# Kernel tuning notes

Hardware: AMD Instinct MI355X
Metric: run time of the kernel (lower is better)

Reference implementation:

```python
import jax, jax.numpy as jnp
import numpy as np

B, N, S, K, CIN = 16, 4096, 1024, 32, 64
EPS = 1e-5


def setup_inputs() -> dict:
    key = jax.random.key(0)
    ks = jax.random.split(key, 6)
    xyz = jax.random.normal(ks[0], (B, N, 3), jnp.float32)
    features = jax.random.normal(ks[1], (B, N, CIN), jnp.float32)
    # random sampling without replacement (mirrors torch.randperm(N)[:npoint])
    fps_idx = jax.vmap(lambda k: jax.random.permutation(k, N)[:S])(
        jax.random.split(ks[2], B)).astype(jnp.int32)
    chans = [CIN + 3, 64, 64, 128]
    params = {}
    for i in range(3):
        cin, cout = chans[i], chans[i + 1]
        params[f"W{i}"] = jax.random.normal(ks[3 + i], (cout, cin), jnp.float32) / np.sqrt(cin).astype(np.float32)
        params[f"b{i}"] = jnp.zeros((cout,), jnp.float32)
        params[f"g{i}"] = jnp.ones((cout,), jnp.float32)
        params[f"bt{i}"] = jnp.zeros((cout,), jnp.float32)
    return dict(xyz=xyz, features=features, fps_idx=fps_idx, **params)


def _mlp_layer(x, W, b, g, bt):
    # x: (B*S, Cin, K); Conv1d(kernel=1) + BatchNorm1d (training stats) + ReLU
    y = jnp.einsum('oc,bck->bok', W, x) + b[None, :, None]
    mu = y.mean(axis=(0, 2), keepdims=True)
    var = y.var(axis=(0, 2), keepdims=True)  # biased var, as in BN normalization
    y = (y - mu) * jax.lax.rsqrt(var + EPS) * g[None, :, None] + bt[None, :, None]
    return jax.nn.relu(y)


def reference(xyz, features, fps_idx, W0, b0, g0, bt0, W1, b1, g1, bt1, W2, b2, g2, bt2):
    # sample centers: (B, S, 3)
    new_xyz = jnp.take_along_axis(xyz, fps_idx[..., None], axis=1)
    # squared pairwise distances (B, S, N)
    d = (jnp.sum(new_xyz * new_xyz, -1)[..., None]
         + jnp.sum(xyz * xyz, -1)[:, None, :]
         - 2.0 * jnp.einsum('bsd,bnd->bsn', new_xyz, xyz))
    _, idx = jax.lax.top_k(-d, K)  # k nearest -> (B, S, K)
    bidx = jnp.arange(B)[:, None, None]
    g_xyz = xyz[bidx, idx] - new_xyz[:, :, None, :]  # (B, S, K, 3) relative coords
    g_feat = features[bidx, idx]                     # (B, S, K, CIN)
    grouped = jnp.concatenate([g_xyz, g_feat], axis=-1)  # (B, S, K, CIN+3)
    x = grouped.reshape(B * S, K, CIN + 3).transpose(0, 2, 1)  # (B*S, C, K)
    x = _mlp_layer(x, W0, b0, g0, bt0)
    x = _mlp_layer(x, W1, b1, g1, bt1)
    x = _mlp_layer(x, W2, b2, g2, bt2)
    new_features = x.max(axis=-1).reshape(B, S, -1)  # (B, S, 128)
    return new_xyz, new_features
```

## Files before the change

kernel.cpp:

```cpp
#include <hip/hip_runtime.h>
#include <stdint.h>

#define B_   16
#define N_   4096
#define S_   1024
#define K_   32
#define CIN_ 64
#define P_   524288
#define PQ_  16384
#define EPS_ 1e-5f

#define SZ_IDX    ((size_t)P_ * 4)
#define SZ_Y      ((size_t)P_ * 64 * 2)
#define SZ_MX     ((size_t)PQ_ * 128 * 4)
#define OFF_IDX   ((size_t)0)
#define OFF_Y0    (OFF_IDX + SZ_IDX)
#define OFF_Y1    (OFF_Y0 + SZ_Y)
#define OFF_MX    (OFF_Y1 + SZ_Y)
#define OFF_MN    (OFF_MX + SZ_MX)
#define OFF_STATS (OFF_MN + SZ_MX)
#define OFF_FIN   (OFF_STATS + 16384)
#define OFF_FPSC  (OFF_FIN + 2048)
#define WS_NEEDED (OFF_FPSC + (size_t)PQ_ * 4)

typedef unsigned short u16;
typedef short bfrag __attribute__((ext_vector_type(8)));
typedef float f32x4 __attribute__((ext_vector_type(4)));

__device__ __forceinline__ float b2f(unsigned v) {
  return __uint_as_float((v & 0xffffu) << 16);
}
__device__ __forceinline__ u16 f2b(float f) {
  unsigned u = __float_as_uint(f);
  unsigned r = (u + 0x7fffu + ((u >> 16) & 1u)) >> 16;
  return (u16)r;
}
__device__ __forceinline__ unsigned pk2(float a, float b) {
  return (unsigned)f2b(a) | ((unsigned)f2b(b) << 16);
}

__global__ __launch_bounds__(256) void fps_canon_kernel(
    const int* __restrict__ fpsraw, int* __restrict__ fpsc)
{
  __shared__ int is64;
  const int tid = threadIdx.x;
  if (tid == 0) is64 = 1;
  __syncthreads();
  if (tid < 64) {
    if (fpsraw[2 * tid + 1] != 0) atomicAnd(&is64, 0);
  }
  __syncthreads();
  int i = blockIdx.x * 256 + tid;
  if (i < PQ_) {
    int src = is64 ? (2 * i) : i;
    int v = fpsraw[src];
    fpsc[i] = (v & 0xFFF);
  }
}

#define NBIN 2048
#define CAND_CAP 512

__global__ __launch_bounds__(256) void knn_kernel(
    const float* __restrict__ xyz, const int* __restrict__ fps,
    int* __restrict__ idxout, float* __restrict__ out_xyz)
{
  __shared__ unsigned hist[NBIN];
  __shared__ float cd[CAND_CAP];
  __shared__ int   ci_[CAND_CAP];
  __shared__ int   sel[K_];
  __shared__ int   wtot[4];
  __shared__ int   sCnt, sCand, sT;

  const int q   = blockIdx.x;
  const int b   = q >> 10;
  const int tid = threadIdx.x;
  const float* xb = xyz + (size_t)b * N_ * 3;
  const int ctr = fps[q];
  const float cx = xb[ctr*3+0], cy = xb[ctr*3+1], cz = xb[ctr*3+2];

  if (tid == 0) {
    out_xyz[(size_t)q*3+0] = cx;
    out_xyz[(size_t)q*3+1] = cy;
    out_xyz[(size_t)q*3+2] = cz;
    sCnt = 0; sCand = 0;
  }
  for (int i = tid; i < NBIN; i += 256) hist[i] = 0u;
  const float s1 = __fadd_rn(__fadd_rn(__fmul_rn(cx,cx), __fmul_rn(cy,cy)), __fmul_rn(cz,cz));
  __syncthreads();

  float dreg[16];
  #pragma unroll
  for (int it = 0; it < 16; ++it) {
    int n = it * 256 + tid;
    float x0 = xb[n*3+0], x1 = xb[n*3+1], x2 = xb[n*3+2];
    float s2 = __fadd_rn(__fadd_rn(__fmul_rn(x0,x0), __fmul_rn(x1,x1)), __fmul_rn(x2,x2));
    float dt = __fadd_rn(__fadd_rn(__fmul_rn(cx,x0), __fmul_rn(cy,x1)), __fmul_rn(cz,x2));
    float d  = __fsub_rn(__fadd_rn(s1, s2), __fmul_rn(2.0f, dt));
    dreg[it] = d;
    float dc = fmaxf(d, 0.0f);
    int bin = (int)(dc * 128.0f); bin = bin > (NBIN-1) ? (NBIN-1) : bin;
    atomicAdd(&hist[bin], 1u);
  }
  __syncthreads();

  const int base = tid * 8;
  int h[8]; int lsum = 0;
  #pragma unroll
  for (int j = 0; j < 8; ++j) { h[j] = (int)hist[base + j]; lsum += h[j]; }
  const int lane = tid & 63, wid = tid >> 6;
  int scv = lsum;
  #pragma unroll
  for (int off = 1; off < 64; off <<= 1) {
    int v = __shfl_up(scv, off, 64);
    if (lane >= off) scv += v;
  }
  if (lane == 63) wtot[wid] = scv;
  __syncthreads();
  int woff = 0;
  for (int w = 0; w < wid; ++w) woff += wtot[w];
  int run = woff + scv - lsum;
  #pragma unroll
  for (int j = 0; j < 8; ++j) {
    int c = h[j];
    if (run < K_ && run + c >= K_) { sT = base + j; }
    run += c;
  }
  __syncthreads();
  const int T = sT;

  const unsigned long long lmask = (lane == 63) ? 0x7fffffffffffffffull
                                                : ((1ull << lane) - 1ull);
  #pragma unroll
  for (int it = 0; it < 16; ++it) {
    int n = it * 256 + tid;
    float d = dreg[it];
    float dc = fmaxf(d, 0.0f);
    int bin = (int)(dc * 128.0f); bin = bin > (NBIN-1) ? (NBIN-1) : bin;
    bool isSel  = (bin < T);
    bool isCand = (bin == T);
    unsigned long long mSel  = __ballot(isSel);
    unsigned long long mCand = __ballot(isCand);
    int baseS = 0, baseC = 0;
    if (lane == 0) {
      if (mSel)  baseS = atomicAdd(&sCnt,  __popcll(mSel));
      if (mCand) baseC = atomicAdd(&sCand, __popcll(mCand));
    }
    baseS = __shfl(baseS, 0, 64);
    baseC = __shfl(baseC, 0, 64);
    if (isSel) {
      int s = baseS + __popcll(mSel & lmask);
      if (s < K_) sel[s] = n;
    }
    if (isCand) {
      int s = baseC + __popcll(mCand & lmask);
      if (s < CAND_CAP) { cd[s] = d; ci_[s] = n; }
    }
  }
  __syncthreads();

  if (wid == 0) {
    int m = sCnt; m = m > K_ ? K_ : m;
    int cc = sCand; cc = cc > CAND_CAP ? CAND_CAP : cc;
    const int r = K_ - m;
    for (int it = 0; it < r; ++it) {
      float bd = 3.0e38f; int bi = 0x7fffffff;
      for (int j = lane; j < cc; j += 64) {
        float dv = cd[j]; int iv = ci_[j];
        if (dv < bd || (dv == bd && iv < bi)) { bd = dv; bi = iv; }
      }
      #pragma unroll
      for (int off = 32; off > 0; off >>= 1) {
        float od = __shfl_down(bd, off, 64);
        int   oi = __shfl_down(bi, off, 64);
        if (od < bd || (od == bd && oi < bi)) { bd = od; bi = oi; }
      }
      int win = __shfl(bi, 0, 64);
      if (lane == 0) sel[m + it] = win & 0xFFF;
      for (int j = lane; j < cc; j += 64) if (ci_[j] == win) cd[j] = 3.0e38f;
    }
  }
  __syncthreads();
  if (tid < K_) idxout[(size_t)q * K_ + tid] = sel[tid] & 0xFFF;
}


__global__ __launch_bounds__(256) void l0_mfma(
    const float* __restrict__ xyz, const float* __restrict__ feat,
    const int* __restrict__ fps, const int* __restrict__ idxin,
    const float* __restrict__ W0, const float* __restrict__ b0,
    uint4* __restrict__ Y0g, float* __restrict__ sumg, float* __restrict__ sqg)
{
  __shared__ uint4 Wl[12*64];
  __shared__ float bl[64];
  __shared__ float ssum[64], ssq[64];

  const int tid = threadIdx.x;
  const int bid0 = blockIdx.x;
  const int rep = (bid0 & 7) << 9;
  const int bid = (bid0 & 7) * ((int)gridDim.x >> 3) + (bid0 >> 3);
  const int pbase = bid * 128;
  const int q0 = bid * 4;
  const int b = bid >> 8;

  if (tid < 64) { bl[tid] = b0 ? b0[tid] : 0.f; ssum[tid] = 0.f; ssq[tid] = 0.f; }
  for (int u = tid; u < 12*64; u += 256) {
    int kc = u >> 6, o = u & 63;
    unsigned pk[4];
    #pragma unroll
    for (int hh = 0; hh < 4; ++hh) {
      int c0 = kc*8 + hh*2, c1 = c0 + 1;
      float v0 = (c0 < 64) ? W0[o*67 + 3 + c0] : (c0 < 67 ? W0[o*67 + (c0-64)] : 0.f);
      float v1 = (c1 < 64) ? W0[o*67 + 3 + c1] : (c1 < 67 ? W0[o*67 + (c1-64)] : 0.f);
      pk[hh] = pk2(v0, v1);
    }
    Wl[u] = make_uint4(pk[0], pk[1], pk[2], pk[3]);
  }

  const int lane = tid & 63, w = tid >> 6, g = lane >> 4, fr = lane & 15;
  const float* xb = xyz + (size_t)b * N_ * 3;
  const float* fbase = feat + (size_t)b * N_ * 64;

  int pidx[2];
  const int ct = fps[q0 + w] & 0xFFF;
  #pragma unroll
  for (int pm = 0; pm < 2; ++pm)
    pidx[pm] = idxin[pbase + w*32 + pm*16 + fr] & 0xFFF;

  bfrag xv[3][2];
  #pragma unroll
  for (int kk = 0; kk < 3; ++kk) {
    const int kc = kk*4 + g;
    #pragma unroll
    for (int pm = 0; pm < 2; ++pm) {
      uint4 uu;
      if (kc < 8) {
        const float* fp = fbase + pidx[pm]*64 + kc*8;
        float4 fa = *(const float4*)fp;
        float4 fb2 = *(const float4*)(fp + 4);
        uu = make_uint4(pk2(fa.x, fa.y), pk2(fa.z, fa.w),
                        pk2(fb2.x, fb2.y), pk2(fb2.z, fb2.w));
      } else if (kc == 8) {
        int n = pidx[pm];
        float dx = xb[n*3+0] - xb[ct*3+0];
        float dy = xb[n*3+1] - xb[ct*3+1];
        float dz = xb[n*3+2] - xb[ct*3+2];
        uu = make_uint4(pk2(dx, dy), (unsigned)f2b(dz), 0u, 0u);
      } else {
        uu = make_uint4(0u, 0u, 0u, 0u);
      }
      xv[kk][pm] = *(bfrag*)&uu;
    }
  }
  __syncthreads();

  f32x4 acc[4][2];
  #pragma unroll
  for (int m = 0; m < 4; ++m)
    #pragma unroll
    for (int j = 0; j < 4; ++j) {
      float v = bl[m*16 + g*4 + j];
      acc[m][0][j] = v; acc[m][1][j] = v;
    }
  #pragma unroll
  for (int kk = 0; kk < 3; ++kk) {
    const int kc = kk*4 + g;
    bfrag a[4];
    #pragma unroll
    for (int m = 0; m < 4; ++m) { uint4 u = Wl[kc*64 + m*16 + fr]; a[m] = *(bfrag*)&u; }
    #pragma unroll
    for (int m = 0; m < 4; ++m)
      #pragma unroll
      for (int pm = 0; pm < 2; ++pm)
        acc[m][pm] = __builtin_amdgcn_mfma_f32_16x16x32_bf16(a[m], xv[kk][pm], acc[m][pm], 0, 0, 0);
  }

  #pragma unroll
  for (int m = 0; m < 4; ++m) {
    #pragma unroll
    for (int j = 0; j < 4; ++j) {
      float v0 = acc[m][0][j], v1 = acc[m][1][j];
      float s = v0 + v1, s2 = v0*v0 + v1*v1;
      #pragma unroll
      for (int d = 1; d < 16; d <<= 1) { s += __shfl_xor(s, d); s2 += __shfl_xor(s2, d); }
      if (fr == 0) {
        atomicAdd(&ssum[m*16 + g*4 + j], s);
        atomicAdd(&ssq[m*16 + g*4 + j], s2);
      }
    }
    #pragma unroll
    for (int pm = 0; pm < 2; ++pm) {
      unsigned lo = pk2(acc[m][pm][0], acc[m][pm][1]);
      unsigned hi = pk2(acc[m][pm][2], acc[m][pm][3]);
      unsigned plo = (unsigned)__shfl_xor((int)lo, 16, 64);
      unsigned phi = (unsigned)__shfl_xor((int)hi, 16, 64);
      if ((g & 1) == 0) {
        size_t unit = (size_t)(m*2 + (g>>1)) * P_ + pbase + w*32 + pm*16 + fr;
        Y0g[unit] = make_uint4(lo, hi, plo, phi);
      }
    }
  }
  __syncthreads();
  if (tid < 64) { atomicAdd(&sumg[rep + tid], ssum[tid]); atomicAdd(&sqg[rep + tid], ssq[tid]); }
}

__global__ __launch_bounds__(256) void l1_mfma(
    const uint4* __restrict__ Y0g,
    const float* __restrict__ W1, const float* __restrict__ b1,
    const float* __restrict__ sc0, const float* __restrict__ sh0,
    uint4* __restrict__ Y1g, float* __restrict__ sumg, float* __restrict__ sqg)
{
  __shared__ uint4 Wl[8*64];
  __shared__ float scl[64], shl[64], bl[64];
  __shared__ float ssum[64], ssq[64];

  const int tid = threadIdx.x;
  const int bid0 = blockIdx.x;
  const int rep = (bid0 & 7) << 9;
  const int bid = (bid0 & 7) * ((int)gridDim.x >> 3) + (bid0 >> 3);
  const int pbase = bid * 128;

  if (tid < 64) {
    scl[tid] = sc0[tid]; shl[tid] = sh0[tid];
    bl[tid] = b1 ? b1[tid] : 0.f;
    ssum[tid] = 0.f; ssq[tid] = 0.f;
  }
  for (int u = tid; u < 8*64; u += 256) {
    int kc = u >> 6, o = u & 63;
    const float* wp = W1 + o*64 + kc*8;
    float4 wa = *(const float4*)wp;
    float4 wb = *(const float4*)(wp + 4);
    Wl[u] = make_uint4(pk2(wa.x, wa.y), pk2(wa.z, wa.w), pk2(wb.x, wb.y), pk2(wb.z, wb.w));
  }
  __syncthreads();

  const int lane = tid & 63, w = tid >> 6, g = lane >> 4, fr = lane & 15;

  bfrag xv[2][2];
  #pragma unroll
  for (int kk = 0; kk < 2; ++kk) {
    const int kc = kk*4 + g;
    float4 sa = *(const float4*)&scl[kc*8];
    float4 sb = *(const float4*)&scl[kc*8 + 4];
    float4 ha = *(const float4*)&shl[kc*8];
    float4 hb = *(const float4*)&shl[kc*8 + 4];
    #pragma unroll
    for (int pm = 0; pm < 2; ++pm) {
      uint4 yv = Y0g[(size_t)kc * P_ + pbase + w*32 + pm*16 + fr];
      unsigned r0 = pk2(fmaxf(fmaf(sa.x, b2f(yv.x),       ha.x), 0.f),
                        fmaxf(fmaf(sa.y, b2f(yv.x >> 16), ha.y), 0.f));
      unsigned r1 = pk2(fmaxf(fmaf(sa.z, b2f(yv.y),       ha.z), 0.f),
                        fmaxf(fmaf(sa.w, b2f(yv.y >> 16), ha.w), 0.f));
      unsigned r2 = pk2(fmaxf(fmaf(sb.x, b2f(yv.z),       hb.x), 0.f),
                        fmaxf(fmaf(sb.y, b2f(yv.z >> 16), hb.y), 0.f));
      unsigned r3 = pk2(fmaxf(fmaf(sb.z, b2f(yv.w),       hb.z), 0.f),
                        fmaxf(fmaf(sb.w, b2f(yv.w >> 16), hb.w), 0.f));
      uint4 uu = make_uint4(r0, r1, r2, r3);
      xv[kk][pm] = *(bfrag*)&uu;
    }
  }

  f32x4 acc[4][2];
  #pragma unroll
  for (int m = 0; m < 4; ++m)
    #pragma unroll
    for (int j = 0; j < 4; ++j) {
      float v = bl[m*16 + g*4 + j];
      acc[m][0][j] = v; acc[m][1][j] = v;
    }
  #pragma unroll
  for (int kk = 0; kk < 2; ++kk) {
    const int kc = kk*4 + g;
    bfrag a[4];
    #pragma unroll
    for (int m = 0; m < 4; ++m) { uint4 u = Wl[kc*64 + m*16 + fr]; a[m] = *(bfrag*)&u; }
    #pragma unroll
    for (int m = 0; m < 4; ++m)
      #pragma unroll
      for (int pm = 0; pm < 2; ++pm)
        acc[m][pm] = __builtin_amdgcn_mfma_f32_16x16x32_bf16(a[m], xv[kk][pm], acc[m][pm], 0, 0, 0);
  }

  #pragma unroll
  for (int m = 0; m < 4; ++m) {
    #pragma unroll
    for (int j = 0; j < 4; ++j) {
      float v0 = acc[m][0][j], v1 = acc[m][1][j];
      float s = v0 + v1, s2 = v0*v0 + v1*v1;
      #pragma unroll
      for (int d = 1; d < 16; d <<= 1) { s += __shfl_xor(s, d); s2 += __shfl_xor(s2, d); }
      if (fr == 0) {
        atomicAdd(&ssum[m*16 + g*4 + j], s);
        atomicAdd(&ssq[m*16 + g*4 + j], s2);
      }
    }
    #pragma unroll
    for (int pm = 0; pm < 2; ++pm) {
      unsigned lo = pk2(acc[m][pm][0], acc[m][pm][1]);
      unsigned hi = pk2(acc[m][pm][2], acc[m][pm][3]);
      unsigned plo = (unsigned)__shfl_xor((int)lo, 16, 64);
      unsigned phi = (unsigned)__shfl_xor((int)hi, 16, 64);
      if ((g & 1) == 0) {
        size_t unit = (size_t)(m*2 + (g>>1)) * P_ + pbase + w*32 + pm*16 + fr;
        Y1g[unit] = make_uint4(lo, hi, plo, phi);
      }
    }
  }
  __syncthreads();
  if (tid < 64) { atomicAdd(&sumg[rep + tid], ssum[tid]); atomicAdd(&sqg[rep + tid], ssq[tid]); }
}

__global__ __launch_bounds__(256) void l2_mfma(
    const uint4* __restrict__ Y1g,
    const float* __restrict__ W2, const float* __restrict__ b2,
    const float* __restrict__ sc1, const float* __restrict__ sh1,
    float* __restrict__ mxg, float* __restrict__ mng,
    float* __restrict__ sumg, float* __restrict__ sqg)
{
  __shared__ uint4 Wl[8*128];
  __shared__ float scl[64], shl[64], bl[128];
  __shared__ float ssum[128], ssq[128];

  const int tid = threadIdx.x;
  const int bid0 = blockIdx.x;
  const int rep = (bid0 & 7) << 9;
  const int bid = (bid0 & 7) * ((int)gridDim.x >> 3) + (bid0 >> 3);
  const int pbase = bid * 128;
  const int q0 = bid * 4;

  if (tid < 64) { scl[tid] = sc1[tid]; shl[tid] = sh1[tid]; }
  if (tid < 128) { bl[tid] = b2 ? b2[tid] : 0.f; ssum[tid] = 0.f; ssq[tid] = 0.f; }
  for (int u = tid; u < 8*128; u += 256) {
    int kc = u >> 7, o = u & 127;
    const float* wp = W2 + o*64 + kc*8;
    float4 wa = *(const float4*)wp;
    float4 wb = *(const float4*)(wp + 4);
    Wl[u] = make_uint4(pk2(wa.x, wa.y), pk2(wa.z, wa.w), pk2(wb.x, wb.y), pk2(wb.z, wb.w));
  }
  __syncthreads();

  const int lane = tid & 63, w = tid >> 6, g = lane >> 4, fr = lane & 15;

  bfrag ax[2][2];
  #pragma unroll
  for (int kk = 0; kk < 2; ++kk) {
    const int kc = kk*4 + g;
    float4 sa = *(const float4*)&scl[kc*8];
    float4 sb = *(const float4*)&scl[kc*8 + 4];
    float4 ha = *(const float4*)&shl[kc*8];
    float4 hb = *(const float4*)&shl[kc*8 + 4];
    #pragma unroll
    for (int pm = 0; pm < 2; ++pm) {
      uint4 yv = Y1g[(size_t)kc * P_ + pbase + w*32 + pm*16 + fr];
      unsigned r0 = pk2(fmaxf(fmaf(sa.x, b2f(yv.x),       ha.x), 0.f),
                        fmaxf(fmaf(sa.y, b2f(yv.x >> 16), ha.y), 0.f));
      unsigned r1 = pk2(fmaxf(fmaf(sa.z, b2f(yv.y),       ha.z), 0.f),
                        fmaxf(fmaf(sa.w, b2f(yv.y >> 16), ha.w), 0.f));
      unsigned r2 = pk2(fmaxf(fmaf(sb.x, b2f(yv.z),       hb.x), 0.f),
                        fmaxf(fmaf(sb.y, b2f(yv.z >> 16), hb.y), 0.f));
      unsigned r3 = pk2(fmaxf(fmaf(sb.z, b2f(yv.w),       hb.z), 0.f),
                        fmaxf(fmaf(sb.w, b2f(yv.w >> 16), hb.w), 0.f));
      uint4 uu = make_uint4(r0, r1, r2, r3);
      ax[kk][pm] = *(bfrag*)&uu;
    }
  }

  f32x4 acc[2][8];
  #pragma unroll
  for (int cn = 0; cn < 8; ++cn) {
    float v = bl[cn*16 + fr];
    #pragma unroll
    for (int j = 0; j < 4; ++j) { acc[0][cn][j] = v; acc[1][cn][j] = v; }
  }
  #pragma unroll
  for (int kk = 0; kk < 2; ++kk) {
    const int kc = kk*4 + g;
    #pragma unroll
    for (int cn = 0; cn < 8; ++cn) {
      uint4 u = Wl[kc*128 + cn*16 + fr];
      bfrag bw = *(bfrag*)&u;
      acc[0][cn] = __builtin_amdgcn_mfma_f32_16x16x32_bf16(ax[kk][0], bw, acc[0][cn], 0, 0, 0);
      acc[1][cn] = __builtin_amdgcn_mfma_f32_16x16x32_bf16(ax[kk][1], bw, acc[1][cn], 0, 0, 0);
    }
  }

  #pragma unroll
  for (int cn = 0; cn < 8; ++cn) {
    float mx = -3.0e38f, mn = 3.0e38f, s = 0.f, s2 = 0.f;
    #pragma unroll
    for (int pm = 0; pm < 2; ++pm)
      #pragma unroll
      for (int j = 0; j < 4; ++j) {
        float v = acc[pm][cn][j];
        mx = fmaxf(mx, v); mn = fminf(mn, v);
        s += v; s2 += v*v;
      }
    #pragma unroll
    for (int d = 16; d < 64; d <<= 1) {
      mx = fmaxf(mx, __shfl_xor(mx, d));
      mn = fminf(mn, __shfl_xor(mn, d));
      s  += __shfl_xor(s, d);
      s2 += __shfl_xor(s2, d);
    }
    if (g == 0) {
      int o = cn*16 + fr;
      size_t q = q0 + w;
      mxg[q*128 + o] = mx;
      mng[q*128 + o] = mn;
      atomicAdd(&ssum[o], s);
      atomicAdd(&ssq[o], s2);
    }
  }
  __syncthreads();
  if (tid < 128) { atomicAdd(&sumg[rep + tid], ssum[tid]); atomicAdd(&sqg[rep + tid], ssq[tid]); }
}

__global__ void finalize_kernel(
    const float* __restrict__ sum, const float* __restrict__ sq,
    const float* __restrict__ g, const float* __restrict__ bt,
    float* __restrict__ sc, float* __restrict__ sh, int C)
{
  int c = threadIdx.x;
  if (c < C) {
    float s = 0.f, s2 = 0.f;
    #pragma unroll
    for (int r = 0; r < 8; ++r) { s += sum[r*512 + c]; s2 += sq[r*512 + c]; }
    const float inv = 1.0f / (float)P_;
    float mu = s * inv;
    float var = s2 * inv - mu * mu;
    var = fmaxf(var, 0.f);
    float rr = 1.0f / sqrtf(var + EPS_);
    float gg = g ? g[c] : 1.0f;
    float bb = bt ? bt[c] : 0.0f;
    float sv = gg * rr;
    sc[c] = sv;
    sh[c] = bb - mu * sv;
  }
}

__global__ __launch_bounds__(256) void out_kernel(
    const float* __restrict__ mxg, const float* __restrict__ mng,
    const float* __restrict__ sc2, const float* __restrict__ sh2,
    float* __restrict__ out)
{
  int i = blockIdx.x * 256 + threadIdx.x;
  int o = i & 127;
  float a = sc2[o];
  float v = (a >= 0.f) ? mxg[i] : mng[i];
  float z = fmaxf(fmaf(a, v, sh2[o]), 0.f);
  out[(size_t)PQ_ * 3 + i] = z;
}

extern "C" void kernel_launch(void* const* d_in, const int* in_sizes, int n_in,
                              void* d_out, int out_size, void* d_ws, size_t ws_size,
                              hipStream_t stream)
{
  int i_xyz=-1, i_feat=-1, i_fps=-1, i_w0=-1, i_w1=-1, i_w2=-1;
  for (int i = 0; i < n_in; ++i) {
    switch (in_sizes[i]) {
      case 196608:  i_xyz = i; break;
      case 4194304: i_feat = i; break;
      case 16384:   i_fps = i; break;
      case 4288:    i_w0 = i; break;
      case 4096:    i_w1 = i; break;
      case 8192:    i_w2 = i; break;
      default: break;
    }
  }
  if (i_xyz < 0 || i_feat < 0 || i_fps < 0 || i_w0 < 0 || i_w1 < 0 || i_w2 < 0) return;

  const float* xyz  = (const float*)d_in[i_xyz];
  const float* feat = (const float*)d_in[i_feat];
  const int*   fpsr = (const int*)d_in[i_fps];
  const float* W0 = (const float*)d_in[i_w0];
  const float* W1 = (const float*)d_in[i_w1];
  const float* W2 = (const float*)d_in[i_w2];

  bool canon = (n_in >= 15 && i_xyz==0 && i_feat==1 && i_fps==2 && i_w0==3 &&
                i_w1==7 && i_w2==11 &&
                in_sizes[4]==64 && in_sizes[5]==64 && in_sizes[6]==64 &&
                in_sizes[8]==64 && in_sizes[9]==64 && in_sizes[10]==64 &&
                in_sizes[12]==128 && in_sizes[13]==128 && in_sizes[14]==128);
  const float* b0 = canon ? (const float*)d_in[4]  : nullptr;
  const float* g0 = canon ? (const float*)d_in[5]  : nullptr;
  const float* bt0= canon ? (const float*)d_in[6]  : nullptr;
  const float* b1 = canon ? (const float*)d_in[8]  : nullptr;
  const float* g1 = canon ? (const float*)d_in[9]  : nullptr;
  const float* bt1= canon ? (const float*)d_in[10] : nullptr;
  const float* b2 = canon ? (const float*)d_in[12] : nullptr;
  const float* g2 = canon ? (const float*)d_in[13] : nullptr;
  const float* bt2= canon ? (const float*)d_in[14] : nullptr;

  float* out = (float*)d_out;
  char* ws = (char*)d_ws;
  if (ws_size < WS_NEEDED) return;

  int* idxw = (int*)(ws + OFF_IDX);
  uint4* Y0 = (uint4*)(ws + OFF_Y0);
  uint4* Y1 = (uint4*)(ws + OFF_Y1);
  float* mxg = (float*)(ws + OFF_MX);
  float* mng = (float*)(ws + OFF_MN);
  float* st  = (float*)(ws + OFF_STATS);
  float* fin = (float*)(ws + OFF_FIN);
  int* fpsc  = (int*)(ws + OFF_FPSC);

  hipMemsetAsync(st, 0, 16384, stream);

  fps_canon_kernel<<<(PQ_+255)/256, 256, 0, stream>>>(fpsr, fpsc);

  knn_kernel<<<PQ_, 256, 0, stream>>>(xyz, fpsc, idxw, out);

  l0_mfma<<<P_/128, 256, 0, stream>>>(xyz, feat, fpsc, idxw, W0, b0, Y0, st + 0, st + 64);
  finalize_kernel<<<1, 64, 0, stream>>>(st + 0, st + 64, g0, bt0, fin + 0, fin + 64, 64);

  l1_mfma<<<P_/128, 256, 0, stream>>>(Y0, W1, b1, fin + 0, fin + 64, Y1, st + 128, st + 192);
  finalize_kernel<<<1, 64, 0, stream>>>(st + 128, st + 192, g1, bt1, fin + 128, fin + 192, 64);

  l2_mfma<<<P_/128, 256, 0, stream>>>(Y1, W2, b2, fin + 128, fin + 192, mxg, mng, st + 256, st + 384);
  finalize_kernel<<<1, 128, 0, stream>>>(st + 256, st + 384, g2, bt2, fin + 256, fin + 384, 128);

  out_kernel<<<(PQ_*128)/256, 256, 0, stream>>>(mxg, mng, fin + 256, fin + 384, out);
}
```

Measured before the change: 251.2 us.

## Precompute padded xyz with squared norms and streamline KNN histogram threshold search

Adds a prep kernel that packs each point as a float4 of (x,y,z,|p|^2), so the KNN kernel does one aligned 16-byte load per point and skips recomputing the squared norm for every query. The histogram prefix scan becomes a single-wave chunked scan that stops early once the K-th bin is found. Selection and candidate classification now compare distances against float bin bounds instead of recomputing bin indices, and the wave-level atomics are skipped when a ballot mask is empty. The cost is an extra small launch and workspace buffer, plus a serial wave-0 scan that could be slower if the threshold bin lies far along the histogram.

Result: faster. 242.5 us (-3.5%).

```diff
diff --git a/kernel.cpp b/kernel.cpp
--- a/kernel.cpp
+++ b/kernel.cpp
@@ -21,7 +21,8 @@
 #define OFF_STATS (OFF_MN + SZ_MX)
 #define OFF_FIN   (OFF_STATS + 16384)
 #define OFF_FPSC  (OFF_FIN + 2048)
-#define WS_NEEDED (OFF_FPSC + (size_t)PQ_ * 4)
+#define OFF_PXYZW (OFF_FPSC + (size_t)PQ_ * 4)
+#define WS_NEEDED (OFF_PXYZW + (size_t)B_ * N_ * 16)
 
 typedef unsigned short u16;
 typedef short bfrag __attribute__((ext_vector_type(8)));
@@ -58,26 +59,35 @@
   }
 }
 
+__global__ __launch_bounds__(256) void prep_kernel(
+    const float* __restrict__ xyz, float4* __restrict__ pxyzw)
+{
+  int i = blockIdx.x * 256 + threadIdx.x;
+  float x0 = xyz[i*3+0], x1 = xyz[i*3+1], x2 = xyz[i*3+2];
+  float s2 = __fadd_rn(__fadd_rn(__fmul_rn(x0,x0), __fmul_rn(x1,x1)), __fmul_rn(x2,x2));
+  pxyzw[i] = make_float4(x0, x1, x2, s2);
+}
+
 #define NBIN 2048
 #define CAND_CAP 512
 
 __global__ __launch_bounds__(256) void knn_kernel(
-    const float* __restrict__ xyz, const int* __restrict__ fps,
+    const float4* __restrict__ pxyzw, const int* __restrict__ fps,
     int* __restrict__ idxout, float* __restrict__ out_xyz)
 {
   __shared__ unsigned hist[NBIN];
   __shared__ float cd[CAND_CAP];
   __shared__ int   ci_[CAND_CAP];
   __shared__ int   sel[K_];
-  __shared__ int   wtot[4];
   __shared__ int   sCnt, sCand, sT;
 
   const int q   = blockIdx.x;
   const int b   = q >> 10;
   const int tid = threadIdx.x;
-  const float* xb = xyz + (size_t)b * N_ * 3;
+  const float4* xb4 = pxyzw + (size_t)b * N_;
   const int ctr = fps[q];
-  const float cx = xb[ctr*3+0], cy = xb[ctr*3+1], cz = xb[ctr*3+2];
+  const float4 cv = xb4[ctr];
+  const float cx = cv.x, cy = cv.y, cz = cv.z, s1 = cv.w;
 
   if (tid == 0) {
     out_xyz[(size_t)q*3+0] = cx;
@@ -85,18 +95,20 @@
     out_xyz[(size_t)q*3+2] = cz;
     sCnt = 0; sCand = 0;
   }
-  for (int i = tid; i < NBIN; i += 256) hist[i] = 0u;
-  const float s1 = __fadd_rn(__fadd_rn(__fmul_rn(cx,cx), __fmul_rn(cy,cy)), __fmul_rn(cz,cz));
+  {
+    uint4* hz = (uint4*)hist;
+    hz[tid]       = make_uint4(0,0,0,0);
+    hz[tid + 256] = make_uint4(0,0,0,0);
+  }
   __syncthreads();
 
   float dreg[16];
   #pragma unroll
   for (int it = 0; it < 16; ++it) {
     int n = it * 256 + tid;
-    float x0 = xb[n*3+0], x1 = xb[n*3+1], x2 = xb[n*3+2];
-    float s2 = __fadd_rn(__fadd_rn(__fmul_rn(x0,x0), __fmul_rn(x1,x1)), __fmul_rn(x2,x2));
-    float dt = __fadd_rn(__fadd_rn(__fmul_rn(cx,x0), __fmul_rn(cy,x1)), __fmul_rn(cz,x2));
-    float d  = __fsub_rn(__fadd_rn(s1, s2), __fmul_rn(2.0f, dt));
+    float4 v = xb4[n];
+    float dt = __fadd_rn(__fadd_rn(__fmul_rn(cx,v.x), __fmul_rn(cy,v.y)), __fmul_rn(cz,v.z));
+    float d  = __fsub_rn(__fadd_rn(s1, v.w), __fmul_rn(2.0f, dt));
     dreg[it] = d;
     float dc = fmaxf(d, 0.0f);
     int bin = (int)(dc * 128.0f); bin = bin > (NBIN-1) ? (NBIN-1) : bin;
@@ -104,57 +116,60 @@
   }
   __syncthreads();
 
-  const int base = tid * 8;
-  int h[8]; int lsum = 0;
-  #pragma unroll
-  for (int j = 0; j < 8; ++j) { h[j] = (int)hist[base + j]; lsum += h[j]; }
   const int lane = tid & 63, wid = tid >> 6;
-  int scv = lsum;
-  #pragma unroll
-  for (int off = 1; off < 64; off <<= 1) {
-    int v = __shfl_up(scv, off, 64);
-    if (lane >= off) scv += v;
-  }
-  if (lane == 63) wtot[wid] = scv;
-  __syncthreads();
-  int woff = 0;
-  for (int w = 0; w < wid; ++w) woff += wtot[w];
-  int run = woff + scv - lsum;
-  #pragma unroll
-  for (int j = 0; j < 8; ++j) {
-    int c = h[j];
-    if (run < K_ && run + c >= K_) { sT = base + j; }
-    run += c;
+  if (wid == 0) {
+    int cum = 0, base = 0, found = 0;
+    while (!found && base < NBIN) {
+      int h = (int)hist[base + lane];
+      int pre = h;
+      #pragma unroll
+      for (int off = 1; off < 64; off <<= 1) {
+        int v = __shfl_up(pre, off, 64);
+        if (lane >= off) pre += v;
+      }
+      int tot = __shfl(pre, 63, 64);
+      bool cross = (cum + pre >= K_) && (cum + pre - h < K_);
+      unsigned long long mm = __ballot(cross);
+      if (mm) {
+        if (lane == 0) sT = base + (int)(__ffsll((long long)mm) - 1);
+        found = 1;
+      }
+      cum += tot;
+      base += 64;
+    }
   }
   __syncthreads();
   const int T = sT;
+  const float fT  = (float)T * 0.0078125f;
+  const float fT1 = (T >= NBIN-1) ? 3.0e38f : (float)(T+1) * 0.0078125f;
 
   const unsigned long long lmask = (lane == 63) ? 0x7fffffffffffffffull
                                                 : ((1ull << lane) - 1ull);
   #pragma unroll
   for (int it = 0; it < 16; ++it) {
     int n = it * 256 + tid;
-    float d = dreg[it];
-    float dc = fmaxf(d, 0.0f);
-    int bin = (int)(dc * 128.0f); bin = bin > (NBIN-1) ? (NBIN-1) : bin;
-    bool isSel  = (bin < T);
-    bool isCand = (bin == T);
+    float dc = fmaxf(dreg[it], 0.0f);
+    bool isSel  = dc < fT;
+    bool isCand = !isSel && (dc < fT1);
     unsigned long long mSel  = __ballot(isSel);
     unsigned long long mCand = __ballot(isCand);
-    int baseS = 0, baseC = 0;
-    if (lane == 0) {
-      if (mSel)  baseS = atomicAdd(&sCnt,  __popcll(mSel));
-      if (mCand) baseC = atomicAdd(&sCand, __popcll(mCand));
-    }
-    baseS = __shfl(baseS, 0, 64);
-    baseC = __shfl(baseC, 0, 64);
-    if (isSel) {
-      int s = baseS + __popcll(mSel & lmask);
-      if (s < K_) sel[s] = n;
-    }
-    if (isCand) {
-      int s = baseC + __popcll(mCand & lmask);
-      if (s < CAND_CAP) { cd[s] = d; ci_[s] = n; }
+    if (mSel) {
+      int baseS = 0;
+      if (lane == 0) baseS = atomicAdd(&sCnt, __popcll(mSel));
+      baseS = __shfl(baseS, 0, 64);
+      if (isSel) {
+        int s = baseS + __popcll(mSel & lmask);
+        if (s < K_) sel[s] = n;
+      }
+    }
+    if (mCand) {
+      int baseC = 0;
+      if (lane == 0) baseC = atomicAdd(&sCand, __popcll(mCand));
+      baseC = __shfl(baseC, 0, 64);
+      if (isCand) {
+        int s = baseC + __popcll(mCand & lmask);
+        if (s < CAND_CAP) { cd[s] = dreg[it]; ci_[s] = n; }
+      }
     }
   }
   __syncthreads();
@@ -603,12 +618,14 @@
   float* st  = (float*)(ws + OFF_STATS);
   float* fin = (float*)(ws + OFF_FIN);
   int* fpsc  = (int*)(ws + OFF_FPSC);
+  float4* pxyzw = (float4*)(ws + OFF_PXYZW);
 
   hipMemsetAsync(st, 0, 16384, stream);
 
   fps_canon_kernel<<<(PQ_+255)/256, 256, 0, stream>>>(fpsr, fpsc);
-
-  knn_kernel<<<PQ_, 256, 0, stream>>>(xyz, fpsc, idxw, out);
+  prep_kernel<<<(B_*N_)/256, 256, 0, stream>>>(xyz, pxyzw);
+
+  knn_kernel<<<PQ_, 256, 0, stream>>>(pxyzw, fpsc, idxw, out);
 
   l0_mfma<<<P_/128, 256, 0, stream>>>(xyz, feat, fpsc, idxw, W0, b0, Y0, st + 0, st + 64);
   finalize_kernel<<<1, 64, 0, stream>>>(st + 0, st + 64, g0, bt0, fin + 0, fin + 64, 64);
```
